# Kernel optimization log

Hardware: AMD Instinct MI355X
Metric: run time of the kernel (lower is better)

Reference implementation:

```python
import jax, jax.numpy as jnp
import numpy as np

N = 100000   # nodes
E = 500000   # edges per relation
R = 3        # relations (etypes)
L = 2        # layers
F = 300      # input features
H = 256      # hidden
C = 23       # classes


def setup_inputs() -> dict:
    key = jax.random.key(0)
    ks = jax.random.split(key, 12)
    s = 0.05
    return {
        "x": jax.random.normal(ks[0], (N, F), jnp.float32),
        "edge_src": jax.random.randint(ks[1], (R, E), 0, N, dtype=jnp.int32),
        "edge_dst": jax.random.randint(ks[2], (R, E), 0, N, dtype=jnp.int32),
        "W_feat": jax.random.normal(ks[3], (F, H), jnp.float32) * s,
        "b_feat": jnp.zeros((H,), jnp.float32),
        "g_feat": jnp.ones((H,), jnp.float32),
        "beta_feat": jnp.zeros((H,), jnp.float32),
        "gcn_W": jax.random.normal(ks[4], (L, R, H, H), jnp.float32) * s,
        "gcn_b": jnp.zeros((L, R, H), jnp.float32),
        "skip_W": jax.random.normal(ks[5], (L, H, H), jnp.float32) * s,
        "skip_b": jnp.zeros((L, H), jnp.float32),
        "bn_g": jnp.ones((L, H), jnp.float32),
        "bn_b": jnp.zeros((L, H), jnp.float32),
        "W_c1": jax.random.normal(ks[6], (H, H), jnp.float32) * s,
        "b_c1": jnp.zeros((H,), jnp.float32),
        "g_c": jnp.ones((H,), jnp.float32),
        "beta_c": jnp.zeros((H,), jnp.float32),
        "W_c2": jax.random.normal(ks[7], (H, C), jnp.float32) * s,
        "b_c2": jnp.zeros((C,), jnp.float32),
    }


def _bn(h, g, b):
    # BatchNorm1d, training-mode batch stats (biased var), eps=1e-5
    m = h.mean(0)
    v = jnp.mean((h - m) ** 2, 0)
    return g * (h - m) * jax.lax.rsqrt(v + 1e-5) + b


def _het_forward(x, edge_src, edge_dst, W_feat, b_feat, g_feat, beta_feat,
                 gcn_W, gcn_b, skip_W, skip_b, bn_g, bn_b,
                 W_c1, b_c1, g_c, beta_c, W_c2, b_c2):
    seg = jax.ops.segment_sum
    ones = jnp.ones((E,), jnp.float32)
    # feat_reduce: Linear + BN + ReLU
    h = jax.nn.relu(_bn(x @ W_feat + b_feat, g_feat, beta_feat))  # [N, H]
    for l in range(L):
        h_res = h @ skip_W[l] + skip_b[l]
        rel = []
        for r in range(R):  # per-relation GraphConv (DGL norm='both')
            src, dst = edge_src[r], edge_dst[r]
            dout = jnp.clip(seg(ones, src, num_segments=N), 1.0, None)
            din = jnp.clip(seg(ones, dst, num_segments=N), 1.0, None)
            xs = h * jax.lax.rsqrt(dout)[:, None]          # src-normalize
            m = seg(xs[src], dst, num_segments=N)          # gather-scatter
            m = m * jax.lax.rsqrt(din)[:, None]            # dst-normalize
            rel.append(m @ gcn_W[l, r] + gcn_b[l, r])
        h = jnp.mean(jnp.stack(rel, 0), 0)  # het_combine='mean'
        h = h + h_res
        h = jax.nn.leaky_relu(_bn(h, bn_g[l], bn_b[l]), 0.01)
        # dropout is identity in eval mode
    # classification head
    h = jax.nn.relu(_bn(h @ W_c1 + b_c1, g_c, beta_c))
    return h @ W_c2 + b_c2  # [N, C]


def reference(x, edge_src, edge_dst, W_feat, b_feat, g_feat, beta_feat,
              gcn_W, gcn_b, skip_W, skip_b, bn_g, bn_b,
              W_c1, b_c1, g_c, beta_c, W_c2, b_c2):
    return _het_forward(x, edge_src, edge_dst, W_feat, b_feat, g_feat,
                        beta_feat, gcn_W, gcn_b, skip_W, skip_b, bn_g, bn_b,
                        W_c1, b_c1, g_c, beta_c, W_c2, b_c2)
```

## Files before the change

kernel.cpp:

```cpp
#include <hip/hip_runtime.h>

#define NN 100000
#define EE 500000
#define RR 3
#define LL 2
#define FF 300
#define HH 256
#define CC 23
#define MPAD 100096
#define SCHUNK 2048
#define SNB ((NN + SCHUNK - 1) / SCHUNK)

static inline int cdiv_h(int a, int b) { return (a + b - 1) / b; }

typedef __attribute__((ext_vector_type(8))) short bf16x8;
typedef __attribute__((ext_vector_type(4))) float f32x4;
typedef __attribute__((ext_vector_type(2))) unsigned short u16x2;

__device__ inline unsigned short f2bf(float f) {
    union { float f; unsigned int u; } v; v.f = f;
    unsigned int r = v.u + 0x7fff + ((v.u >> 16) & 1);
    return (unsigned short)(r >> 16);
}
__device__ inline float bf2f(unsigned short u) {
    union { unsigned int u; float f; } v; v.u = ((unsigned int)u) << 16;
    return v.f;
}
__device__ inline void gl_lds16(const void* g, void* l) {
    __builtin_amdgcn_global_load_lds((const __attribute__((address_space(1))) unsigned int*)g,
                                     (__attribute__((address_space(3))) unsigned int*)l,
                                     16, 0, 0);
}

__global__ void hist_kernel(const int* __restrict__ src, const int* __restrict__ dst,
                            int* __restrict__ cnt_out, int* __restrict__ cnt_in,
                            int RE, int Eper) {
    int i = blockIdx.x * blockDim.x + threadIdx.x;
    if (i >= RE) return;
    int r = i / Eper;
    atomicAdd(&cnt_out[r * NN + src[i]], 1);
    atomicAdd(&cnt_in[r * NN + dst[i]], 1);
}

__global__ void rs_kernel(const int* __restrict__ cnt_out, const int* __restrict__ cnt_in,
                          float* __restrict__ rs_out, float* __restrict__ rs_in, int total) {
    int i = blockIdx.x * blockDim.x + threadIdx.x;
    if (i >= total) return;
    rs_out[i] = rsqrtf(fmaxf((float)cnt_out[i], 1.0f));
    rs_in[i]  = rsqrtf(fmaxf((float)cnt_in[i], 1.0f));
}

__global__ __launch_bounds__(256) void scan_a(const int* __restrict__ cnt, int* __restrict__ bsum) {
    int r = blockIdx.y, b = blockIdx.x, t = threadIdx.x;
    const int* c = cnt + (size_t)r * NN;
    int base = b * SCHUNK;
    int s = 0;
    for (int i = t; i < SCHUNK; i += 256) {
        int idx = base + i;
        if (idx < NN) s += c[idx];
    }
#pragma unroll
    for (int o = 1; o < 64; o <<= 1) s += __shfl_xor(s, o);
    __shared__ int sh[4];
    if ((t & 63) == 0) sh[t >> 6] = s;
    __syncthreads();
    if (t == 0) bsum[r * SNB + b] = sh[0] + sh[1] + sh[2] + sh[3];
}

__global__ void scan_b(int* __restrict__ bsum, int* __restrict__ offs) {
    int r = threadIdx.x;
    if (r >= RR) return;
    int* bs = bsum + r * SNB;
    int run = 0;
    for (int i = 0; i < SNB; i++) { int v = bs[i]; bs[i] = run; run += v; }
    offs[(size_t)r * (NN + 1) + NN] = run;
}

__global__ __launch_bounds__(256) void scan_c(const int* __restrict__ cnt, const int* __restrict__ bsum,
                                              int* __restrict__ offs, int* __restrict__ cur) {
    int r = blockIdx.y, b = blockIdx.x, t = threadIdx.x;
    const int* c = cnt + (size_t)r * NN;
    int base = b * SCHUNK + t * 8;
    int v[8]; int s = 0;
#pragma unroll
    for (int j = 0; j < 8; j++) {
        int idx = base + j;
        v[j] = (idx < NN) ? c[idx] : 0;
        s += v[j];
    }
    __shared__ int sh[256];
    sh[t] = s;
    __syncthreads();
    for (int d = 1; d < 256; d <<= 1) {
        int x = (t >= d) ? sh[t - d] : 0;
        __syncthreads();
        sh[t] += x;
        __syncthreads();
    }
    int run = sh[t] - s + bsum[r * SNB + b];
    int* orow = offs + (size_t)r * (NN + 1);
    int* crow = cur + (size_t)r * NN;
#pragma unroll
    for (int j = 0; j < 8; j++) {
        int idx = base + j;
        if (idx < NN) { orow[idx] = run; crow[idx] = run; }
        run += v[j];
    }
}

__global__ void fill_kernel(const int* __restrict__ src, const int* __restrict__ dst,
                            const float* __restrict__ rs_out,
                            int* __restrict__ cur, int2* __restrict__ srcw,
                            int RE, int Eper) {
    int i = blockIdx.x * blockDim.x + threadIdx.x;
    if (i >= RE) return;
    int r = i / Eper;
    int d = dst[i];
    int s = src[i];
    float w = rs_out[r * NN + s];
    int pos = atomicAdd(&cur[r * NN + d], 1);
    srcw[(size_t)r * Eper + pos] = make_int2(s, __float_as_int(w));
}

__global__ __launch_bounds__(256) void convert_x(const float* __restrict__ x, unsigned short* __restrict__ xpad) {
    int idx = blockIdx.x * blockDim.x + threadIdx.x;
    if (idx >= MPAD * 80) return;
    int row = idx / 80, c4 = (idx - row * 80) * 4;
    ushort4 o;
    if (row < NN && c4 + 3 < FF) {
        float4 v = *(const float4*)(x + (size_t)row * FF + c4);
        o.x = f2bf(v.x); o.y = f2bf(v.y); o.z = f2bf(v.z); o.w = f2bf(v.w);
    } else {
        o.x = 0; o.y = 0; o.z = 0; o.w = 0;
    }
    *(ushort4*)(xpad + (size_t)row * 320 + c4) = o;
}

__global__ void wprep_feat(const float* __restrict__ W, unsigned short* __restrict__ Bt) {
    int n = blockIdx.x;
    int k = threadIdx.x;
    float v = (k < FF) ? W[(size_t)k * HH + n] : 0.f;
    Bt[(size_t)n * 320 + k] = f2bf(v);
}

__global__ void wprep_layer(const float* __restrict__ skipW, const float* __restrict__ gcnW,
                            unsigned short* __restrict__ Bt) {
    int idx = blockIdx.x * blockDim.x + threadIdx.x;
    int n = idx >> 10, k = idx & 1023;
    int seg = k >> 8, k2 = k & 255;
    float v = (seg == 0) ? skipW[(size_t)k2 * HH + n]
                         : gcnW[(size_t)(seg - 1) * HH * HH + (size_t)k2 * HH + n] * (1.0f / 3.0f);
    Bt[(size_t)n * 1024 + k] = f2bf(v);
}

__global__ void bias_layer(const float* __restrict__ skip_b, const float* __restrict__ gcn_b,
                           float* __restrict__ bias) {
    int t = threadIdx.x;
    bias[t] = skip_b[t] + (gcn_b[t] + gcn_b[HH + t] + gcn_b[2 * HH + t]) * (1.0f / 3.0f);
}

__global__ void wprep_c1(const float* __restrict__ W, unsigned short* __restrict__ Bt) {
    int idx = blockIdx.x * blockDim.x + threadIdx.x;
    int n = idx >> 8, k = idx & 255;
    Bt[(size_t)n * HH + k] = f2bf(W[(size_t)k * HH + n]);
}

__global__ void wprep_c2(const float* __restrict__ W, unsigned short* __restrict__ Bt) {
    int n = blockIdx.x;
    int k = threadIdx.x;
    float v = (n < CC) ? W[(size_t)k * CC + n] : 0.f;
    Bt[(size_t)n * HH + k] = f2bf(v);
}

__global__ __launch_bounds__(256) void agg_bf16(unsigned short* __restrict__ hcat,
                                                const int* __restrict__ offs_all,
                                                const int2* __restrict__ srcw_all,
                                                const float* __restrict__ rs_in_all,
                                                int half) {
    int r = blockIdx.y;
    const int* offs = offs_all + (size_t)r * (NN + 1);
    const int2* srcw = srcw_all + (size_t)r * EE;
    const float* rs_i = rs_in_all + (size_t)r * NN;
    int wave = threadIdx.x >> 6;
    int lane = threadIdx.x & 63;
    int node = blockIdx.x * 4 + wave;
    if (node >= NN) return;
    int s0 = __builtin_amdgcn_readfirstlane(offs[node]);
    int s1 = __builtin_amdgcn_readfirstlane(offs[node + 1]);
    int cnt = s1 - s0;
    const int2* ew = srcw + s0;
    const unsigned short* hb = hcat + half * 128 + lane * 2;
    float a0 = 0.f, a1 = 0.f;
    int k = 0;
    for (; k + 8 <= cnt; k += 8) {
        int2 e[8];
#pragma unroll
        for (int q = 0; q < 8; q++) e[q] = ew[k + q];
        ushort2 hv[8];
#pragma unroll
        for (int q = 0; q < 8; q++) hv[q] = *(const ushort2*)(hb + (size_t)e[q].x * 1024);
#pragma unroll
        for (int q = 0; q < 8; q++) {
            float u = __int_as_float(e[q].y);
            a0 += u * bf2f(hv[q].x); a1 += u * bf2f(hv[q].y);
        }
    }
    if (k + 4 <= cnt) {
        int2 e[4];
#pragma unroll
        for (int q = 0; q < 4; q++) e[q] = ew[k + q];
        ushort2 hv[4];
#pragma unroll
        for (int q = 0; q < 4; q++) hv[q] = *(const ushort2*)(hb + (size_t)e[q].x * 1024);
#pragma unroll
        for (int q = 0; q < 4; q++) {
            float u = __int_as_float(e[q].y);
            a0 += u * bf2f(hv[q].x); a1 += u * bf2f(hv[q].y);
        }
        k += 4;
    }
    int rem = cnt - k;
    if (rem > 0) {
        int2 e[3];
#pragma unroll
        for (int q = 0; q < 3; q++) {
            int kk = k + q; if (kk > cnt - 1) kk = cnt - 1;
            e[q] = ew[kk];
        }
        ushort2 hv[3];
#pragma unroll
        for (int q = 0; q < 3; q++) hv[q] = *(const ushort2*)(hb + (size_t)e[q].x * 1024);
        float u0 = __int_as_float(e[0].y);
        float u1 = rem > 1 ? __int_as_float(e[1].y) : 0.f;
        float u2 = rem > 2 ? __int_as_float(e[2].y) : 0.f;
        a0 += u0 * bf2f(hv[0].x) + u1 * bf2f(hv[1].x) + u2 * bf2f(hv[2].x);
        a1 += u0 * bf2f(hv[0].y) + u1 * bf2f(hv[1].y) + u2 * bf2f(hv[2].y);
    }
    float wi = rs_i[node];
    u16x2 o;
    o.x = f2bf(a0 * wi); o.y = f2bf(a1 * wi);
    __builtin_nontemporal_store(o, (u16x2*)(hcat + (size_t)node * 1024 + 256 * (r + 1) + half * 128 + lane * 2));
}

__global__ __launch_bounds__(512, 4) void mfma_gemm(const unsigned short* __restrict__ A, int ldA,
                                                    const unsigned short* __restrict__ Bt,
                                                    const float* __restrict__ bias,
                                                    void* __restrict__ Cv, int ldC,
                                                    int Nstore, int K, int c_bf16,
                                                    float* __restrict__ stats) {
    __shared__ unsigned short lds[33792];
    int tid = threadIdx.x;
    int w = tid >> 6, lane = tid & 63;
    int quad = lane >> 4, lr = lane & 15;
    int bm = blockIdx.y * 128;
    int wm = w >> 2, wn = w & 3;
    int lrow = lane >> 2;
    int lslot = lane & 3;

    f32x4 acc[4][4];
#pragma unroll
    for (int i = 0; i < 4; i++)
#pragma unroll
        for (int j = 0; j < 4; j++) acc[i][j] = (f32x4){0.f, 0.f, 0.f, 0.f};

    for (int k0 = 0; k0 < K; k0 += 64) {
        int rA = w * 16 + lrow;
        int cgA = lslot ^ ((rA >> 1) & 3);
#pragma unroll
        for (int h = 0; h < 2; h++) {
            gl_lds16(A + (size_t)(bm + rA) * ldA + k0 + h * 32 + cgA * 8,
                     &lds[h * 4096 + w * 512]);
#pragma unroll
            for (int c = 0; c < 2; c++) {
                int cc = w * 2 + c;
                int rB = cc * 16 + lrow;
                int cgB = lslot ^ ((rB >> 1) & 3);
                gl_lds16(Bt + (size_t)rB * K + k0 + h * 32 + cgB * 8,
                         &lds[8192 + h * 8192 + cc * 512]);
            }
        }
        __syncthreads();
#pragma unroll
        for (int h = 0; h < 2; h++) {
            bf16x8 af[4], bfr[4];
#pragma unroll
            for (int i = 0; i < 4; i++) {
                int r = wm * 64 + i * 16 + lr;
                int s = quad ^ ((r >> 1) & 3);
                af[i] = *(const bf16x8*)&lds[h * 4096 + r * 32 + s * 8];
            }
#pragma unroll
            for (int j = 0; j < 4; j++) {
                int n = wn * 64 + j * 16 + lr;
                int s = quad ^ ((n >> 1) & 3);
                bfr[j] = *(const bf16x8*)&lds[8192 + h * 8192 + n * 32 + s * 8];
            }
#pragma unroll
            for (int i = 0; i < 4; i++)
#pragma unroll
                for (int j = 0; j < 4; j++)
                    acc[i][j] = __builtin_amdgcn_mfma_f32_16x16x32_bf16(af[i], bfr[j], acc[i][j], 0, 0, 0);
        }
        __syncthreads();
    }

    if (c_bf16) {
        unsigned short* ldsC = lds;
#pragma unroll
        for (int j = 0; j < 4; j++) {
            int col = wn * 64 + j * 16 + lr;
            float bv = bias ? bias[col] : 0.f;
            float ssum = 0.f, ssq = 0.f;
#pragma unroll
            for (int i = 0; i < 4; i++) {
#pragma unroll
                for (int v = 0; v < 4; v++) {
                    int row = wm * 64 + i * 16 + quad * 4 + v;
                    float val = acc[i][j][v] + bv;
                    ldsC[row * 264 + col] = f2bf(val);
                    if (bm + row < NN) { ssum += val; ssq += val * val; }
                }
            }
            if (stats) {
                ssum += __shfl_xor(ssum, 16); ssum += __shfl_xor(ssum, 32);
                ssq  += __shfl_xor(ssq, 16);  ssq  += __shfl_xor(ssq, 32);
                if (quad == 0) {
                    atomicAdd(&stats[col], ssum);
                    atomicAdd(&stats[HH + col], ssq);
                }
            }
        }
        __syncthreads();
        int row = tid >> 2, seg = tid & 3;
        if (bm + row < NN) {
            const unsigned short* srcp = ldsC + row * 264 + seg * 64;
            unsigned short* dstp = (unsigned short*)Cv + (size_t)(bm + row) * ldC + seg * 64;
#pragma unroll
            for (int q = 0; q < 8; q++)
                *(uint4*)(dstp + q * 8) = *(const uint4*)(srcp + q * 8);
        }
    } else {
        float* Cf = (float*)Cv;
#pragma unroll
        for (int j = 0; j < 4; j++) {
            int col = wn * 64 + j * 16 + lr;
            if (col >= Nstore) continue;
            float bv = bias ? bias[col] : 0.f;
#pragma unroll
            for (int i = 0; i < 4; i++) {
#pragma unroll
                for (int v = 0; v < 4; v++) {
                    int row = bm + wm * 64 + i * 16 + quad * 4 + v;
                    if (row < NN) Cf[(size_t)row * ldC + col] = acc[i][j][v] + bv;
                }
            }
        }
    }
}

__global__ void bn_coef(const float* __restrict__ stats, const float* __restrict__ g,
                        const float* __restrict__ b, float* __restrict__ coef, float invM) {
    int c = threadIdx.x;
    float mean = stats[c] * invM;
    float var = stats[HH + c] * invM - mean * mean;
    float inv = rsqrtf(var + 1e-5f);
    float sc = g[c] * inv;
    coef[c] = sc;
    coef[HH + c] = b[c] - mean * sc;
}

__global__ __launch_bounds__(256) void bn_apply_v(const unsigned short* __restrict__ Z,
                                                  const float* __restrict__ coef,
                                                  unsigned short* __restrict__ out, int act) {
    int idx = blockIdx.x * blockDim.x + threadIdx.x;
    if (idx >= NN * 32) return;
    int row = idx >> 5, cg = (idx & 31) * 8;
    union { uint4 u; unsigned short s[8]; } zin, zo;
    zin.u = *(const uint4*)(Z + (size_t)row * HH + cg);
    f32x4 sc0 = *(const f32x4*)(coef + cg);
    f32x4 sc1 = *(const f32x4*)(coef + cg + 4);
    f32x4 sh0 = *(const f32x4*)(coef + HH + cg);
    f32x4 sh1 = *(const f32x4*)(coef + HH + cg + 4);
#pragma unroll
    for (int j = 0; j < 8; j++) {
        float sc = (j < 4) ? sc0[j] : sc1[j - 4];
        float sh = (j < 4) ? sh0[j] : sh1[j - 4];
        float v = bf2f(zin.s[j]) * sc + sh;
        if (act == 1) v = fmaxf(v, 0.f);
        else v = (v < 0.f) ? 0.01f * v : v;
        zo.s[j] = f2bf(v);
    }
    *(uint4*)(out + (size_t)row * 1024 + cg) = zo.u;
}

extern "C" void kernel_launch(void* const* d_in, const int* in_sizes, int n_in,
                              void* d_out, int out_size, void* d_ws, size_t ws_size,
                              hipStream_t stream) {
    const float* x        = (const float*)d_in[0];
    const int*   esrc     = (const int*)d_in[1];
    const int*   edst     = (const int*)d_in[2];
    const float* W_feat   = (const float*)d_in[3];
    const float* b_feat   = (const float*)d_in[4];
    const float* g_feat   = (const float*)d_in[5];
    const float* beta_feat= (const float*)d_in[6];
    const float* gcn_W    = (const float*)d_in[7];
    const float* gcn_b    = (const float*)d_in[8];
    const float* skip_W   = (const float*)d_in[9];
    const float* skip_b   = (const float*)d_in[10];
    const float* bn_g     = (const float*)d_in[11];
    const float* bn_b     = (const float*)d_in[12];
    const float* W_c1     = (const float*)d_in[13];
    const float* b_c1     = (const float*)d_in[14];
    const float* g_c      = (const float*)d_in[15];
    const float* beta_c   = (const float*)d_in[16];
    const float* W_c2     = (const float*)d_in[17];
    const float* b_c2     = (const float*)d_in[18];
    float* out = (float*)d_out;
    (void)in_sizes; (void)n_in; (void)out_size; (void)ws_size;

    char* w = (char*)d_ws;
    size_t off = 0;
    auto alloc = [&](size_t bytes) { void* p = w + off; off += (bytes + 255) & ~(size_t)255; return p; };
    unsigned short* hcat = (unsigned short*)alloc((size_t)MPAD * 1024 * 2);
    unsigned short* xpad = hcat;
    unsigned short* c_acc = (unsigned short*)alloc((size_t)NN * HH * 2);
    float* f_stats = (float*)alloc(4 * 2 * HH * 4);
    float* f_coef  = (float*)alloc(2 * HH * 4);
    float* f_rs_out = (float*)alloc((size_t)RR * NN * 4);
    float* f_rs_in  = (float*)alloc((size_t)RR * NN * 4);
    int* i_cnt_out = (int*)alloc((size_t)RR * NN * 4);
    int* i_cnt_in  = (int*)alloc((size_t)RR * NN * 4);
    int* i_off     = (int*)alloc((size_t)RR * (NN + 1) * 4);
    int* i_cur     = (int*)alloc((size_t)RR * NN * 4);
    int2* i_srcw   = (int2*)alloc((size_t)RR * EE * 8);
    int* i_bsum    = (int*)alloc((size_t)RR * SNB * 4);
    unsigned short* Bt_feat = (unsigned short*)alloc(256 * 320 * 2);
    unsigned short* Bt_l0   = (unsigned short*)alloc(256 * 1024 * 2);
    unsigned short* Bt_l1   = (unsigned short*)alloc(256 * 1024 * 2);
    unsigned short* Bt_c1   = (unsigned short*)alloc(256 * 256 * 2);
    unsigned short* Bt_c2   = (unsigned short*)alloc(256 * 256 * 2);
    float* bias_l0 = (float*)alloc(HH * 4);
    float* bias_l1 = (float*)alloc(HH * 4);

    const float invM = 1.0f / (float)NN;
    const int RE = RR * EE;

    (void)hipMemsetAsync(i_cnt_out, 0, (size_t)RR * NN * 4, stream);
    (void)hipMemsetAsync(i_cnt_in, 0, (size_t)RR * NN * 4, stream);
    (void)hipMemsetAsync(f_stats, 0, 4 * 2 * HH * 4, stream);
    hist_kernel<<<cdiv_h(RE, 256), 256, 0, stream>>>(esrc, edst, i_cnt_out, i_cnt_in, RE, EE);
    rs_kernel<<<cdiv_h(RR * NN, 256), 256, 0, stream>>>(i_cnt_out, i_cnt_in, f_rs_out, f_rs_in, RR * NN);
    scan_a<<<dim3(SNB, RR), 256, 0, stream>>>(i_cnt_in, i_bsum);
    scan_b<<<1, 64, 0, stream>>>(i_bsum, i_off);
    scan_c<<<dim3(SNB, RR), 256, 0, stream>>>(i_cnt_in, i_bsum, i_off, i_cur);
    fill_kernel<<<cdiv_h(RE, 256), 256, 0, stream>>>(esrc, edst, f_rs_out, i_cur, i_srcw, RE, EE);

    convert_x<<<cdiv_h(MPAD * 80, 256), 256, 0, stream>>>(x, xpad);
    wprep_feat<<<256, 320, 0, stream>>>(W_feat, Bt_feat);
    wprep_layer<<<1024, 256, 0, stream>>>(skip_W, gcn_W, Bt_l0);
    wprep_layer<<<1024, 256, 0, stream>>>(skip_W + (size_t)HH * HH, gcn_W + (size_t)RR * HH * HH, Bt_l1);
    bias_layer<<<1, 256, 0, stream>>>(skip_b, gcn_b, bias_l0);
    bias_layer<<<1, 256, 0, stream>>>(skip_b + HH, gcn_b + (size_t)RR * HH, bias_l1);
    wprep_c1<<<256, 256, 0, stream>>>(W_c1, Bt_c1);
    wprep_c2<<<256, 256, 0, stream>>>(W_c2, Bt_c2);

    dim3 grid_G(1, MPAD / 128);
    dim3 grid_A(cdiv_h(NN, 4), RR);
    const int nblk_a = cdiv_h(NN * 32, 256);
    float* st0 = f_stats;
    float* st1 = f_stats + 2 * HH;
    float* st2 = f_stats + 4 * HH;
    float* st3 = f_stats + 6 * HH;

    mfma_gemm<<<grid_G, 512, 0, stream>>>(xpad, 320, Bt_feat, b_feat, c_acc, HH, HH, 320, 1, st0);
    bn_coef<<<1, 256, 0, stream>>>(st0, g_feat, beta_feat, f_coef, invM);
    bn_apply_v<<<nblk_a, 256, 0, stream>>>(c_acc, f_coef, hcat, 1);

    for (int l = 0; l < LL; l++) {
        agg_bf16<<<grid_A, 256, 0, stream>>>(hcat, i_off, i_srcw, f_rs_in, 0);
        agg_bf16<<<grid_A, 256, 0, stream>>>(hcat, i_off, i_srcw, f_rs_in, 1);
        float* st = l ? st2 : st1;
        mfma_gemm<<<grid_G, 512, 0, stream>>>(hcat, 1024, l ? Bt_l1 : Bt_l0,
                                              l ? bias_l1 : bias_l0, c_acc, HH, HH, 1024, 1, st);
        bn_coef<<<1, 256, 0, stream>>>(st, bn_g + (size_t)l * HH, bn_b + (size_t)l * HH, f_coef, invM);
        bn_apply_v<<<nblk_a, 256, 0, stream>>>(c_acc, f_coef, hcat, 2);
    }

    mfma_gemm<<<grid_G, 512, 0, stream>>>(hcat, 1024, Bt_c1, b_c1, c_acc, HH, HH, 256, 1, st3);
    bn_coef<<<1, 256, 0, stream>>>(st3, g_c, beta_c, f_coef, invM);
    bn_apply_v<<<nblk_a, 256, 0, stream>>>(c_acc, f_coef, hcat + 256, 1);
    mfma_gemm<<<grid_G, 512, 0, stream>>>(hcat + 256, 1024, Bt_c2, b_c2, out, CC, CC, 256, 0, nullptr);
}
```

Before: 1.232 ms.

## Use LDS-chunked histogram and CSR fill; merge aggregation halves into one pass

Degree counting and CSR construction now use shared-memory histograms and cursors per 16K-node chunk, replacing global atomics, and the separate cursor array is removed. The two half-width aggregation launches are merged into one launch that gathers 4 bf16 values per lane, so edge lists are read once. The fill kernel launches only 21 blocks, each scanning all edges of its relation, so low parallelism may offset the cheaper atomics.

Result: slower. 1.898 ms (+54.0%).

```diff
diff --git a/kernel.cpp b/kernel.cpp
--- a/kernel.cpp
+++ b/kernel.cpp
@@ -10,12 +10,15 @@
 #define MPAD 100096
 #define SCHUNK 2048
 #define SNB ((NN + SCHUNK - 1) / SCHUNK)
+#define CH 16384
+#define NCHUNK 7
+#define HES 4
 
 static inline int cdiv_h(int a, int b) { return (a + b - 1) / b; }
 
 typedef __attribute__((ext_vector_type(8))) short bf16x8;
 typedef __attribute__((ext_vector_type(4))) float f32x4;
-typedef __attribute__((ext_vector_type(2))) unsigned short u16x2;
+typedef __attribute__((ext_vector_type(4))) unsigned short u16x4;
 
 __device__ inline unsigned short f2bf(float f) {
     union { float f; unsigned int u; } v; v.f = f;
@@ -32,14 +35,35 @@
                                      16, 0, 0);
 }
 
-__global__ void hist_kernel(const int* __restrict__ src, const int* __restrict__ dst,
-                            int* __restrict__ cnt_out, int* __restrict__ cnt_in,
-                            int RE, int Eper) {
-    int i = blockIdx.x * blockDim.x + threadIdx.x;
-    if (i >= RE) return;
-    int r = i / Eper;
-    atomicAdd(&cnt_out[r * NN + src[i]], 1);
-    atomicAdd(&cnt_in[r * NN + dst[i]], 1);
+__global__ __launch_bounds__(256) void hist_lds(const int* __restrict__ esrc,
+                                                const int* __restrict__ edst,
+                                                int* __restrict__ cnt_out,
+                                                int* __restrict__ cnt_in) {
+    __shared__ unsigned int h[CH];
+    int chunk = blockIdx.x, r = blockIdx.y;
+    int dir = blockIdx.z >> 2, es = blockIdx.z & 3;
+    const int* ids = (dir ? edst : esrc) + (size_t)r * EE;
+    int* cnt = (dir ? cnt_in : cnt_out) + (size_t)r * NN;
+    int base = chunk * CH;
+    for (int j = threadIdx.x; j < CH; j += 256) h[j] = 0;
+    __syncthreads();
+    const int lo4 = es * (EE / HES / 4), hi4 = lo4 + EE / HES / 4;
+    const int4* ids4 = (const int4*)ids;
+    for (int i = lo4 + threadIdx.x; i < hi4; i += 256) {
+        int4 v = ids4[i];
+        unsigned o0 = (unsigned)(v.x - base), o1 = (unsigned)(v.y - base);
+        unsigned o2 = (unsigned)(v.z - base), o3 = (unsigned)(v.w - base);
+        if (o0 < CH) atomicAdd(&h[o0], 1u);
+        if (o1 < CH) atomicAdd(&h[o1], 1u);
+        if (o2 < CH) atomicAdd(&h[o2], 1u);
+        if (o3 < CH) atomicAdd(&h[o3], 1u);
+    }
+    __syncthreads();
+    for (int j = threadIdx.x; j < CH; j += 256) {
+        unsigned v = h[j];
+        int idx = base + j;
+        if (v && idx < NN) atomicAdd(&cnt[idx], (int)v);
+    }
 }
 
 __global__ void rs_kernel(const int* __restrict__ cnt_out, const int* __restrict__ cnt_in,
@@ -77,7 +101,7 @@
 }
 
 __global__ __launch_bounds__(256) void scan_c(const int* __restrict__ cnt, const int* __restrict__ bsum,
-                                              int* __restrict__ offs, int* __restrict__ cur) {
+                                              int* __restrict__ offs) {
     int r = blockIdx.y, b = blockIdx.x, t = threadIdx.x;
     const int* c = cnt + (size_t)r * NN;
     int base = b * SCHUNK + t * 8;
@@ -99,27 +123,46 @@
     }
     int run = sh[t] - s + bsum[r * SNB + b];
     int* orow = offs + (size_t)r * (NN + 1);
-    int* crow = cur + (size_t)r * NN;
 #pragma unroll
     for (int j = 0; j < 8; j++) {
         int idx = base + j;
-        if (idx < NN) { orow[idx] = run; crow[idx] = run; }
+        if (idx < NN) orow[idx] = run;
         run += v[j];
     }
 }
 
-__global__ void fill_kernel(const int* __restrict__ src, const int* __restrict__ dst,
-                            const float* __restrict__ rs_out,
-                            int* __restrict__ cur, int2* __restrict__ srcw,
-                            int RE, int Eper) {
-    int i = blockIdx.x * blockDim.x + threadIdx.x;
-    if (i >= RE) return;
-    int r = i / Eper;
-    int d = dst[i];
-    int s = src[i];
-    float w = rs_out[r * NN + s];
-    int pos = atomicAdd(&cur[r * NN + d], 1);
-    srcw[(size_t)r * Eper + pos] = make_int2(s, __float_as_int(w));
+__global__ __launch_bounds__(256) void fill_lds(const int* __restrict__ esrc,
+                                                const int* __restrict__ edst,
+                                                const float* __restrict__ rs_out,
+                                                const int* __restrict__ offs_all,
+                                                int2* __restrict__ srcw) {
+    __shared__ int curL[CH];
+    int chunk = blockIdx.x, r = blockIdx.y;
+    int base = chunk * CH;
+    const int* offs = offs_all + (size_t)r * (NN + 1);
+    for (int j = threadIdx.x; j < CH; j += 256) {
+        int idx = base + j;
+        curL[j] = (idx < NN) ? offs[idx] : 0;
+    }
+    __syncthreads();
+    const int4* s4p = (const int4*)(esrc + (size_t)r * EE);
+    const int4* d4p = (const int4*)(edst + (size_t)r * EE);
+    const float* rso = rs_out + (size_t)r * NN;
+    int2* out = srcw + (size_t)r * EE;
+    for (int i = threadIdx.x; i < EE / 4; i += 256) {
+        int4 d4 = d4p[i];
+        int4 s4 = s4p[i];
+#pragma unroll
+        for (int q = 0; q < 4; q++) {
+            int d = (q == 0) ? d4.x : (q == 1) ? d4.y : (q == 2) ? d4.z : d4.w;
+            unsigned off = (unsigned)(d - base);
+            if (off < CH) {
+                int s = (q == 0) ? s4.x : (q == 1) ? s4.y : (q == 2) ? s4.z : s4.w;
+                int pos = atomicAdd(&curL[off], 1);
+                out[pos] = make_int2(s, __float_as_int(rso[s]));
+            }
+        }
+    }
 }
 
 __global__ __launch_bounds__(256) void convert_x(const float* __restrict__ x, unsigned short* __restrict__ xpad) {
@@ -175,8 +218,7 @@
 __global__ __launch_bounds__(256) void agg_bf16(unsigned short* __restrict__ hcat,
                                                 const int* __restrict__ offs_all,
                                                 const int2* __restrict__ srcw_all,
-                                                const float* __restrict__ rs_in_all,
-                                                int half) {
+                                                const float* __restrict__ rs_in_all) {
     int r = blockIdx.y;
     const int* offs = offs_all + (size_t)r * (NN + 1);
     const int2* srcw = srcw_all + (size_t)r * EE;
@@ -189,33 +231,35 @@
     int s1 = __builtin_amdgcn_readfirstlane(offs[node + 1]);
     int cnt = s1 - s0;
     const int2* ew = srcw + s0;
-    const unsigned short* hb = hcat + half * 128 + lane * 2;
-    float a0 = 0.f, a1 = 0.f;
+    const unsigned short* hb = hcat + lane * 4;
+    float a0 = 0.f, a1 = 0.f, a2 = 0.f, a3 = 0.f;
     int k = 0;
     for (; k + 8 <= cnt; k += 8) {
         int2 e[8];
 #pragma unroll
         for (int q = 0; q < 8; q++) e[q] = ew[k + q];
-        ushort2 hv[8];
-#pragma unroll
-        for (int q = 0; q < 8; q++) hv[q] = *(const ushort2*)(hb + (size_t)e[q].x * 1024);
+        ushort4 hv[8];
+#pragma unroll
+        for (int q = 0; q < 8; q++) hv[q] = *(const ushort4*)(hb + (size_t)e[q].x * 1024);
 #pragma unroll
         for (int q = 0; q < 8; q++) {
             float u = __int_as_float(e[q].y);
             a0 += u * bf2f(hv[q].x); a1 += u * bf2f(hv[q].y);
+            a2 += u * bf2f(hv[q].z); a3 += u * bf2f(hv[q].w);
         }
     }
     if (k + 4 <= cnt) {
         int2 e[4];
 #pragma unroll
         for (int q = 0; q < 4; q++) e[q] = ew[k + q];
-        ushort2 hv[4];
-#pragma unroll
-        for (int q = 0; q < 4; q++) hv[q] = *(const ushort2*)(hb + (size_t)e[q].x * 1024);
+        ushort4 hv[4];
+#pragma unroll
+        for (int q = 0; q < 4; q++) hv[q] = *(const ushort4*)(hb + (size_t)e[q].x * 1024);
 #pragma unroll
         for (int q = 0; q < 4; q++) {
             float u = __int_as_float(e[q].y);
             a0 += u * bf2f(hv[q].x); a1 += u * bf2f(hv[q].y);
+            a2 += u * bf2f(hv[q].z); a3 += u * bf2f(hv[q].w);
         }
         k += 4;
     }
@@ -227,19 +271,22 @@
             int kk = k + q; if (kk > cnt - 1) kk = cnt - 1;
             e[q] = ew[kk];
         }
-        ushort2 hv[3];
-#pragma unroll
-        for (int q = 0; q < 3; q++) hv[q] = *(const ushort2*)(hb + (size_t)e[q].x * 1024);
+        ushort4 hv[3];
+#pragma unroll
+        for (int q = 0; q < 3; q++) hv[q] = *(const ushort4*)(hb + (size_t)e[q].x * 1024);
         float u0 = __int_as_float(e[0].y);
         float u1 = rem > 1 ? __int_as_float(e[1].y) : 0.f;
         float u2 = rem > 2 ? __int_as_float(e[2].y) : 0.f;
         a0 += u0 * bf2f(hv[0].x) + u1 * bf2f(hv[1].x) + u2 * bf2f(hv[2].x);
         a1 += u0 * bf2f(hv[0].y) + u1 * bf2f(hv[1].y) + u2 * bf2f(hv[2].y);
+        a2 += u0 * bf2f(hv[0].z) + u1 * bf2f(hv[1].z) + u2 * bf2f(hv[2].z);
+        a3 += u0 * bf2f(hv[0].w) + u1 * bf2f(hv[1].w) + u2 * bf2f(hv[2].w);
     }
     float wi = rs_i[node];
-    u16x2 o;
+    u16x4 o;
     o.x = f2bf(a0 * wi); o.y = f2bf(a1 * wi);
-    __builtin_nontemporal_store(o, (u16x2*)(hcat + (size_t)node * 1024 + 256 * (r + 1) + half * 128 + lane * 2));
+    o.z = f2bf(a2 * wi); o.w = f2bf(a3 * wi);
+    __builtin_nontemporal_store(o, (u16x4*)(hcat + (size_t)node * 1024 + 256 * (r + 1) + lane * 4));
 }
 
 __global__ __launch_bounds__(512, 4) void mfma_gemm(const unsigned short* __restrict__ A, int ldA,
@@ -431,7 +478,6 @@
     int* i_cnt_out = (int*)alloc((size_t)RR * NN * 4);
     int* i_cnt_in  = (int*)alloc((size_t)RR * NN * 4);
     int* i_off     = (int*)alloc((size_t)RR * (NN + 1) * 4);
-    int* i_cur     = (int*)alloc((size_t)RR * NN * 4);
     int2* i_srcw   = (int2*)alloc((size_t)RR * EE * 8);
     int* i_bsum    = (int*)alloc((size_t)RR * SNB * 4);
     unsigned short* Bt_feat = (unsigned short*)alloc(256 * 320 * 2);
@@ -443,17 +489,16 @@
     float* bias_l1 = (float*)alloc(HH * 4);
 
     const float invM = 1.0f / (float)NN;
-    const int RE = RR * EE;
 
     (void)hipMemsetAsync(i_cnt_out, 0, (size_t)RR * NN * 4, stream);
     (void)hipMemsetAsync(i_cnt_in, 0, (size_t)RR * NN * 4, stream);
     (void)hipMemsetAsync(f_stats, 0, 4 * 2 * HH * 4, stream);
-    hist_kernel<<<cdiv_h(RE, 256), 256, 0, stream>>>(esrc, edst, i_cnt_out, i_cnt_in, RE, EE);
+    hist_lds<<<dim3(NCHUNK, RR, 2 * HES), 256, 0, stream>>>(esrc, edst, i_cnt_out, i_cnt_in);
     rs_kernel<<<cdiv_h(RR * NN, 256), 256, 0, stream>>>(i_cnt_out, i_cnt_in, f_rs_out, f_rs_in, RR * NN);
     scan_a<<<dim3(SNB, RR), 256, 0, stream>>>(i_cnt_in, i_bsum);
     scan_b<<<1, 64, 0, stream>>>(i_bsum, i_off);
-    scan_c<<<dim3(SNB, RR), 256, 0, stream>>>(i_cnt_in, i_bsum, i_off, i_cur);
-    fill_kernel<<<cdiv_h(RE, 256), 256, 0, stream>>>(esrc, edst, f_rs_out, i_cur, i_srcw, RE, EE);
+    scan_c<<<dim3(SNB, RR), 256, 0, stream>>>(i_cnt_in, i_bsum, i_off);
+    fill_lds<<<dim3(NCHUNK, RR), 256, 0, stream>>>(esrc, edst, f_rs_out, i_off, i_srcw);
 
     convert_x<<<cdiv_h(MPAD * 80, 256), 256, 0, stream>>>(x, xpad);
     wprep_feat<<<256, 320, 0, stream>>>(W_feat, Bt_feat);
@@ -477,8 +522,7 @@
     bn_apply_v<<<nblk_a, 256, 0, stream>>>(c_acc, f_coef, hcat, 1);
 
     for (int l = 0; l < LL; l++) {
-        agg_bf16<<<grid_A, 256, 0, stream>>>(hcat, i_off, i_srcw, f_rs_in, 0);
-        agg_bf16<<<grid_A, 256, 0, stream>>>(hcat, i_off, i_srcw, f_rs_in, 1);
+        agg_bf16<<<grid_A, 256, 0, stream>>>(hcat, i_off, i_srcw, f_rs_in);
         float* st = l ? st2 : st1;
         mfma_gemm<<<grid_G, 512, 0, stream>>>(hcat, 1024, l ? Bt_l1 : Bt_l0,
                                               l ? bias_l1 : bias_l0, c_acc, HH, HH, 1024, 1, st);
```
